# Kernel optimization log

Measured on AMD Instinct MI355X. Metric: run time of the kernel, lower is better.

The kernel has to match this reference:

```python
import jax, jax.numpy as jnp
import numpy as np

N_NODES = 100000
D_FEAT = 128
N_EDGES = 625000


def setup_inputs() -> dict:
    key = jax.random.key(0)
    k1, k2, k3 = jax.random.split(key, 3)
    ds_in = jax.random.normal(k1, (N_NODES, D_FEAT), dtype=jnp.float32)
    ds_out = jax.random.normal(k2, (N_NODES, D_FEAT), dtype=jnp.float32)
    layer_edge_index = jax.random.randint(k3, (2, N_EDGES), 0, N_NODES, dtype=jnp.int64)
    return {"ds_in": ds_in, "ds_out": ds_out, "layer_edge_index": layer_edge_index}


def reference(ds_in, ds_out, layer_edge_index):
    # out[v] = (ds_out[v] + sum_{edges (v <- u)} ds_in[u]) / (1 + in_degree(v))
    recv = layer_edge_index[0]
    src = layer_edge_index[1]
    n = ds_out.shape[0]
    msg_sum = jax.ops.segment_sum(ds_in[src], recv, num_segments=n)  # [N, D]
    deg = jax.ops.segment_sum(jnp.ones(recv.shape, dtype=ds_out.dtype), recv, num_segments=n)  # [N]
    return (ds_out + msg_sum) / (deg + 1.0)[:, None]
```

## Files before the change

### kernel.cpp

```cpp
#include <hip/hip_runtime.h>

#define N_NODES 100000
#define D_FEAT  128
#define N_EDGES 625000

__global__ void build_links_kernel(const int* __restrict__ recv,
                                   int* __restrict__ head,
                                   int* __restrict__ next) {
    int e = blockIdx.x * blockDim.x + threadIdx.x;
    if (e >= N_EDGES) return;
    int r = recv[e];
    next[e] = atomicExch(&head[r], e);
}

__global__ void gather_kernel(const float4* __restrict__ ds_in4,
                              const float4* __restrict__ ds_out4,
                              const int* __restrict__ head,
                              const int* __restrict__ next,
                              const int* __restrict__ src,
                              float4* __restrict__ out4) {
    int node = blockIdx.x * 8 + (threadIdx.x >> 5);
    int lane = threadIdx.x & 31;
    if (node >= N_NODES) return;

    float4 acc = ds_out4[node * 32 + lane];
    int d = 0;
    int e = head[node];
    while (e >= 0) {
        int en = next[e];
        int s  = src[e];
        float4 v = ds_in4[s * 32 + lane];
        acc.x += v.x; acc.y += v.y; acc.z += v.z; acc.w += v.w;
        d++;
        e = en;
    }
    float inv = 1.0f / (1.0f + (float)d);
    acc.x *= inv; acc.y *= inv; acc.z *= inv; acc.w *= inv;
    out4[node * 32 + lane] = acc;
}

extern "C" void kernel_launch(void* const* d_in, const int* in_sizes, int n_in,
                              void* d_out, int out_size, void* d_ws, size_t ws_size,
                              hipStream_t stream) {
    const float* ds_in  = (const float*)d_in[0];
    const float* ds_out = (const float*)d_in[1];
    const int*   eidx   = (const int*)d_in[2];
    const int* recv = eidx;
    const int* src  = eidx + N_EDGES;
    float* out = (float*)d_out;

    int* head = (int*)d_ws;
    int* next = head + N_NODES;

    hipMemsetAsync(head, 0xFF, N_NODES * sizeof(int), stream);

    build_links_kernel<<<(N_EDGES + 255) / 256, 256, 0, stream>>>(recv, head, next);

    gather_kernel<<<(N_NODES + 7) / 8, 256, 0, stream>>>(
        (const float4*)ds_in, (const float4*)ds_out, head, next, src, (float4*)out);
}
```

Measured before the change: 217.3 us.

## Fuse edge bucketing and gather into one persistent kernel with grid barriers

Result: slower. 463.3 us (+113.2%).

```diff
diff --git a/kernel.cpp b/kernel.cpp
--- a/kernel.cpp
+++ b/kernel.cpp
@@ -4,39 +4,137 @@
 #define D_FEAT  128
 #define N_EDGES 625000
 
-__global__ void build_links_kernel(const int* __restrict__ recv,
-                                   int* __restrict__ head,
-                                   int* __restrict__ next) {
-    int e = blockIdx.x * blockDim.x + threadIdx.x;
-    if (e >= N_EDGES) return;
-    int r = recv[e];
-    next[e] = atomicExch(&head[r], e);
+#define NBLK  256
+#define NTHR  1024
+#define NPB   391
+#define CAP   3072
+#define CHUNK 2442
+
+typedef float vfloat4 __attribute__((ext_vector_type(4)));
+
+#define MAGIC(k) (0x5EED0C00 + (k))
+
+__device__ __forceinline__ void grid_barrier(int* flags, int k) {
+    __syncthreads();
+    if (threadIdx.x == 0) {
+        __threadfence();
+        __hip_atomic_store(&flags[k * NBLK + blockIdx.x], MAGIC(k),
+                           __ATOMIC_RELEASE, __HIP_MEMORY_SCOPE_AGENT);
+    }
+    if (threadIdx.x < NBLK) {
+        while (__hip_atomic_load(&flags[k * NBLK + threadIdx.x],
+                                 __ATOMIC_ACQUIRE, __HIP_MEMORY_SCOPE_AGENT) != MAGIC(k)) {
+            __builtin_amdgcn_s_sleep(1);
+        }
+    }
+    __syncthreads();
+    __threadfence();
 }
 
-__global__ void gather_kernel(const float4* __restrict__ ds_in4,
-                              const float4* __restrict__ ds_out4,
-                              const int* __restrict__ head,
-                              const int* __restrict__ next,
-                              const int* __restrict__ src,
-                              float4* __restrict__ out4) {
-    int node = blockIdx.x * 8 + (threadIdx.x >> 5);
-    int lane = threadIdx.x & 31;
-    if (node >= N_NODES) return;
+__global__ __launch_bounds__(NTHR) void fused_kernel(
+    const int* __restrict__ recv, const int* __restrict__ src,
+    const vfloat4* __restrict__ ds_in4, const vfloat4* __restrict__ ds_out4,
+    vfloat4* __restrict__ out4,
+    int* __restrict__ counts,
+    int* __restrict__ packed,
+    int* __restrict__ flags)
+{
+    __shared__ int smem[22528];
+    const int t = threadIdx.x;
+    const int b = blockIdx.x;
 
-    float4 acc = ds_out4[node * 32 + lane];
-    int d = 0;
-    int e = head[node];
-    while (e >= 0) {
-        int en = next[e];
-        int s  = src[e];
-        float4 v = ds_in4[s * 32 + lane];
-        acc.x += v.x; acc.y += v.y; acc.z += v.z; acc.w += v.w;
-        d++;
-        e = en;
+    if (t < 3)
+        __hip_atomic_store(&flags[t * NBLK + b], 0, __ATOMIC_RELAXED, __HIP_MEMORY_SCOPE_AGENT);
+
+    int* hist = smem;
+    if (t < 256) hist[t] = 0;
+    __syncthreads();
+    const int cbeg = b * CHUNK;
+    const int cend = min(cbeg + CHUNK, N_EDGES);
+    for (int i = cbeg + t; i < cend; i += NTHR)
+        atomicAdd(&hist[recv[i] / NPB], 1);
+    __syncthreads();
+    if (t < 256) counts[t * NBLK + b] = hist[t];
+
+    grid_barrier(flags, 0);
+
+    int* tmp = smem;
+    int v = 0;
+    if (t < 256) { v = counts[b * NBLK + t]; tmp[t] = v; }
+    __syncthreads();
+    for (int off = 1; off < 256; off <<= 1) {
+        int x = 0;
+        if (t < 256 && t >= off) x = tmp[t - off];
+        __syncthreads();
+        if (t < 256) tmp[t] += x;
+        __syncthreads();
     }
-    float inv = 1.0f / (1.0f + (float)d);
-    acc.x *= inv; acc.y *= inv; acc.z *= inv; acc.w *= inv;
-    out4[node * 32 + lane] = acc;
+    if (t < 256) counts[b * NBLK + t] = tmp[t] - v;
+    if (t == 255) smem[22000] = tmp[255];
+
+    grid_barrier(flags, 1);
+
+    int* cur = smem;
+    if (t < 256) cur[t] = t * CAP + counts[t * NBLK + b];
+    __syncthreads();
+    for (int i = cbeg + t; i < cend; i += NTHR) {
+        int r  = recv[i];
+        int s  = src[i];
+        int bk = r / NPB;
+        int pos = atomicAdd(&cur[bk], 1);
+        packed[pos] = ((r - bk * NPB) << 17) | s;
+    }
+
+    grid_barrier(flags, 2);
+
+    const int cnt = smem[22000];
+    int* cnt_lds = smem;
+    int* excl    = smem + 512;
+    int* cursor  = smem + 1024;
+    int* pk_lds  = smem + 2048;
+    int* ssrc_l  = smem + 2048 + CAP;
+    if (t < 512) cnt_lds[t] = 0;
+    __syncthreads();
+    for (int i = t; i < cnt; i += NTHR) {
+        int pk = packed[b * CAP + i];
+        pk_lds[i] = pk;
+        atomicAdd(&cnt_lds[pk >> 17], 1);
+    }
+    __syncthreads();
+    int v2 = 0;
+    if (t < 512) { v2 = cnt_lds[t]; excl[t] = v2; }
+    __syncthreads();
+    for (int off = 1; off < 512; off <<= 1) {
+        int x = 0;
+        if (t < 512 && t >= off) x = excl[t - off];
+        __syncthreads();
+        if (t < 512) excl[t] += x;
+        __syncthreads();
+    }
+    if (t < 512) { excl[t] -= v2; cursor[t] = excl[t]; }
+    __syncthreads();
+    for (int i = t; i < cnt; i += NTHR) {
+        int pk = pk_lds[i];
+        int slot = atomicAdd(&cursor[pk >> 17], 1);
+        ssrc_l[slot] = pk & 0x1FFFF;
+    }
+    __syncthreads();
+
+    const int g = t >> 5, lane = t & 31;
+    for (int ln = g; ln < NPB; ln += 32) {
+        int node = b * NPB + ln;
+        if (node >= N_NODES) break;
+        int beg = excl[ln];
+        int d   = cnt_lds[ln];
+        vfloat4 acc = __builtin_nontemporal_load(&ds_out4[node * 32 + lane]);
+        for (int k = 0; k < d; k++) {
+            int s = ssrc_l[beg + k];
+            acc += ds_in4[s * 32 + lane];
+        }
+        float inv = 1.0f / (1.0f + (float)d);
+        acc *= inv;
+        __builtin_nontemporal_store(acc, &out4[node * 32 + lane]);
+    }
 }
 
 extern "C" void kernel_launch(void* const* d_in, const int* in_sizes, int n_in,
@@ -49,13 +147,11 @@
     const int* src  = eidx + N_EDGES;
     float* out = (float*)d_out;
 
-    int* head = (int*)d_ws;
-    int* next = head + N_NODES;
+    int* counts = (int*)d_ws;
+    int* packed = counts + NBLK * NBLK;
+    int* flags  = packed + NBLK * CAP;
 
-    hipMemsetAsync(head, 0xFF, N_NODES * sizeof(int), stream);
-
-    build_links_kernel<<<(N_EDGES + 255) / 256, 256, 0, stream>>>(recv, head, next);
-
-    gather_kernel<<<(N_NODES + 7) / 8, 256, 0, stream>>>(
-        (const float4*)ds_in, (const float4*)ds_out, head, next, src, (float4*)out);
+    fused_kernel<<<NBLK, NTHR, 0, stream>>>(
+        recv, src, (const vfloat4*)ds_in, (const vfloat4*)ds_out, (vfloat4*)out,
+        counts, packed, flags);
 }
```
